# Kernel optimization log

Hardware: AMD Instinct MI355X
Metric: run time of the kernel (lower is better)

## Reference

```python
import jax, jax.numpy as jnp
import numpy as np

D_MODEL = 1024
NUM_HEADS = 16
D_K = D_MODEL // NUM_HEADS
HEADS_DIST = [4, 4, 2, 2, 4]  # [token, statement, data_flow, control_flow, standard]
HYP_DF = 5.0
HYP_CF = 5.0
NEG_INF = -1000000000.0
B, S = 4, 1024


def _head_group_weights():
    # one-hot-per-group weight vectors of length NUM_HEADS
    ws = []
    start = 0
    for n in HEADS_DIST:
        w = np.zeros(NUM_HEADS, dtype=np.float32)
        w[start:start + n] = 1.0
        ws.append(jnp.asarray(w))
        start += n
    return ws  # tok_w, stmt_w, df_w, cf_w, std_w


def setup_inputs() -> dict:
    key = jax.random.key(0)
    ks = jax.random.split(key, 12)
    f32 = jnp.float32
    inp = {
        'Q': jax.random.normal(ks[0], (B, S, D_MODEL), f32),
        'K': jax.random.normal(ks[1], (B, S, D_MODEL), f32),
        'V': jax.random.normal(ks[2], (B, S, D_MODEL), f32),
        'token': jax.random.randint(ks[3], (B, S, S), 0, 2).astype(f32),
        'statement': jax.random.randint(ks[4], (B, S, S), 0, 2).astype(f32),
        'data_flow': jax.random.randint(ks[5], (B, S, S), 0, 2).astype(f32),
        'control_flow': jax.random.randint(ks[6], (B, S, S), 0, 2).astype(f32),
        'zero_matrix': jnp.zeros((B, S, S), f32),
        'mask': jax.random.randint(ks[7], (B, 1, S, S), 0, 2).astype(jnp.int32),
        # linear layer params (torch nn.Linear: y = x @ W.T + b)
        'Wq': jax.random.normal(ks[8], (D_MODEL, D_MODEL), f32) * 0.02,
        'bq': jnp.zeros((D_MODEL,), f32),
        'Wk': jax.random.normal(ks[9], (D_MODEL, D_MODEL), f32) * 0.02,
        'bk': jnp.zeros((D_MODEL,), f32),
        'Wv': jax.random.normal(ks[10], (D_MODEL, D_MODEL), f32) * 0.02,
        'bv': jnp.zeros((D_MODEL,), f32),
        'Wo': jax.random.normal(ks[11], (D_MODEL, D_MODEL), f32) * 0.02,
        'bo': jnp.zeros((D_MODEL,), f32),
    }
    return inp


def _split_heads(x):
    b, s, _ = x.shape
    return x.reshape(b, s, NUM_HEADS, D_K).transpose(0, 2, 1, 3)  # (B,H,S,dk)


def reference(Q, K, V, token, statement, data_flow, control_flow, zero_matrix,
              mask, Wq, bq, Wk, bk, Wv, bv, Wo, bo):
    tok_w, stmt_w, df_w, cf_w, _ = _head_group_weights()

    Qh = _split_heads(Q @ Wq.T + bq)
    Kh = _split_heads(K @ Wk.T + bk)
    Vh = _split_heads(V @ Wv.T + bv)

    scores = jnp.einsum('bhqd,bhkd->bhqk', Qh, Kh) / jnp.sqrt(jnp.float32(D_K))

    # local mask: -1e9 * token for token-heads, -1e9 * statement for statement-heads,
    # zero_matrix (zeros) elsewhere — expressed via per-head group weights instead of
    # the original redundant stack.
    w = lambda v: v[None, :, None, None]  # (1,H,1,1)
    local_mask = NEG_INF * (w(tok_w) * token[:, None] + w(stmt_w) * statement[:, None])
    # global enhance: |scores * (hyp_df*data_flow | hyp_cf*control_flow)| on their heads
    enhance_adj = (HYP_DF * w(df_w) * data_flow[:, None]
                   + HYP_CF * w(cf_w) * control_flow[:, None])
    global_enhance = jnp.abs(enhance_adj * scores)

    scores = scores + local_mask + global_enhance
    scores = jnp.where(mask == 0, NEG_INF, scores)

    probs = jax.nn.softmax(scores, axis=-1)  # (B,H,S,S)
    ctx = jnp.einsum('bhqk,bhkd->bhqd', probs, Vh)
    out = ctx.transpose(0, 2, 1, 3).reshape(B, S, D_MODEL)
    return out @ Wo.T + bo
```

## Files before the change

kernel.cpp:

```cpp
#include <hip/hip_runtime.h>
#include <stdint.h>

typedef unsigned short u16;
typedef unsigned int   u32;
typedef unsigned char  u8;
typedef __attribute__((ext_vector_type(4))) float f32x4;
typedef __attribute__((ext_vector_type(8))) __bf16 bf16x8;
typedef __attribute__((ext_vector_type(2))) unsigned int u32x2;
typedef __attribute__((ext_vector_type(4))) unsigned int u32x4;

#define MFMA16(a, b, c) __builtin_amdgcn_mfma_f32_16x16x32_bf16((a), (b), (c), 0, 0, 0)

__device__ __forceinline__ u16 f2bf(float f) {
  u32 u = __float_as_uint(f);
  return (u16)((u + 0x7fffu + ((u >> 16) & 1u)) >> 16);
}

__device__ __forceinline__ void gl_lds16(const void* g, void* l) {
  __builtin_amdgcn_global_load_lds((const __attribute__((address_space(1))) u32*)g,
                                   (__attribute__((address_space(3))) u32*)l, 16, 0, 0);
}

__device__ __forceinline__ u32 cvtpk(float a, float b) {
  u32 r;
  asm("v_cvt_pk_bf16_f32 %0, %1, %2" : "=v"(r) : "v"(a), "v"(b));
  return r;
}

__device__ __forceinline__ float exp2_hw(float x) {
  float r;
  asm("v_exp_f32 %0, %1" : "=v"(r) : "v"(x));
  return r;
}

__device__ __forceinline__ void plswap32(u32& x, u32& y) {
  u32x2 r = __builtin_amdgcn_permlane32_swap(x, y, false, false);
  x = r.x; y = r.y;
}
__device__ __forceinline__ void plswap16(u32& x, u32& y) {
  u32x2 r = __builtin_amdgcn_permlane16_swap(x, y, false, false);
  x = r.x; y = r.y;
}

__device__ __forceinline__ float redmax_lg(float v) {
  u32 x = __float_as_uint(v), y = x;
  plswap16(x, y);
  float m = fmaxf(__uint_as_float(x), __uint_as_float(y));
  u32 a = __float_as_uint(m), b = a;
  plswap32(a, b);
  return fmaxf(__uint_as_float(a), __uint_as_float(b));
}
__device__ __forceinline__ float redsum_lg(float v) {
  u32 x = __float_as_uint(v), y = x;
  plswap16(x, y);
  float m = __uint_as_float(x) + __uint_as_float(y);
  u32 a = __float_as_uint(m), b = a;
  plswap32(a, b);
  return __uint_as_float(a) + __uint_as_float(b);
}

__device__ __forceinline__ u32 pbit(float t, float s, float d, float c, int m) {
  const u32 nm = (m == 0) ? 1u : 0u;
  u32 r = (t != 0.0f ? 1u : 0u) | (s != 0.0f ? 2u : 0u) | (d != 0.0f ? 4u : 0u) |
          (c != 0.0f ? 8u : 0u) | ((1u - nm) << 4);
  r |= (((t != 0.0f ? 1u : 0u) | nm) << 5) | (((s != 0.0f ? 1u : 0u) | nm) << 6) | (nm << 7);
  return r;
}

__global__ void __launch_bounds__(256) pack_kernel(const float4* __restrict__ tok, const float4* __restrict__ st,
                                                   const float4* __restrict__ df, const float4* __restrict__ cf,
                                                   const int4* __restrict__ msk, u32* __restrict__ pko) {
  const int i = blockIdx.x * 256 + threadIdx.x;
  const int b = i >> 18, rem = i & 262143, q = rem >> 8, k4 = rem & 255;
  const int t = k4 >> 4, nk = (k4 >> 2) & 3, lg = k4 & 3;
  const u32 widx = ((u32)(b * 64 + (q >> 4)) * 16 + t) * 256 + (q & 15) * 16 + lg * 4 + nk;
  float4 vt = tok[i], vs = st[i], vd = df[i], vc = cf[i];
  int4 vm = msk[i];
  u32 b0 = pbit(vt.x, vs.x, vd.x, vc.x, vm.x);
  u32 b1 = pbit(vt.y, vs.y, vd.y, vc.y, vm.y);
  u32 b2 = pbit(vt.z, vs.z, vd.z, vc.z, vm.z);
  u32 b3 = pbit(vt.w, vs.w, vd.w, vc.w, vm.w);
  pko[widx] = b0 | (b1 << 8) | (b2 << 16) | (b3 << 24);
}

__global__ void __launch_bounds__(256) gemm_qkv(const float* __restrict__ Qf, const float* __restrict__ Kf,
                                                const float* __restrict__ Vf, const float* __restrict__ Wqf,
                                                const float* __restrict__ Wkf, const float* __restrict__ Wvf,
                                                const float* __restrict__ bq, const float* __restrict__ bk,
                                                const float* __restrict__ bv, u16* __restrict__ Obase) {
  __shared__ u16 smA[128 * 32];
  __shared__ u16 smB[128 * 32];
  const int fb = blockIdx.x;
  const int lid = (fb & 7) * 96 + (fb >> 3);
  const int z = lid >> 8;
  const int m0 = ((lid & 255) >> 3) * 128;
  const int n0 = (lid & 7) * 128;
  const float* A = (z == 0) ? Qf : (z == 1) ? Kf : Vf;
  const float* W = (z == 0) ? Wqf : (z == 1) ? Wkf : Wvf;
  const float* bias = (z == 0) ? bq : (z == 1) ? bk : bv;
  u16* Out = Obase + (size_t)z * 4194304;
  const int t = threadIdx.x;
  const int w = t >> 6, l = t & 63;
  const int l15 = l & 15, lg = l >> 4;
  const int wr = w >> 1, wc = w & 1;
  f32x4 acc[4][4] = {};
  const int srow = w * 16 + (l >> 2);
  const int scol = (l & 3) * 8;
  const float* Ab = A + (size_t)(m0 + srow) * 1024 + scol;
  const float* Wb = W + (size_t)(n0 + srow) * 1024 + scol;
  u16* sA0 = smA + srow * 32 + scol;
  u16* sB0 = smB + srow * 32 + scol;

  float4 ra[2][2], rb[2][2];
#pragma unroll
  for (int p = 0; p < 2; p++)
#pragma unroll
    for (int hf = 0; hf < 2; hf++) {
      ra[p][hf] = *(const float4*)(Ab + p * 65536 + hf * 4);
      rb[p][hf] = *(const float4*)(Wb + p * 65536 + hf * 4);
    }

  for (int kk = 0; kk < 1024; kk += 32) {
    __syncthreads();
#pragma unroll
    for (int p = 0; p < 2; p++) {
      u32x4 wa = {cvtpk(ra[p][0].x, ra[p][0].y), cvtpk(ra[p][0].z, ra[p][0].w),
                  cvtpk(ra[p][1].x, ra[p][1].y), cvtpk(ra[p][1].z, ra[p][1].w)};
      *(u32x4*)(sA0 + p * 2048) = wa;
      u32x4 wb2 = {cvtpk(rb[p][0].x, rb[p][0].y), cvtpk(rb[p][0].z, rb[p][0].w),
                   cvtpk(rb[p][1].x, rb[p][1].y), cvtpk(rb[p][1].z, rb[p][1].w)};
      *(u32x4*)(sB0 + p * 2048) = wb2;
    }
    __syncthreads();
    if (kk < 992) {
#pragma unroll
      for (int p = 0; p < 2; p++)
#pragma unroll
        for (int hf = 0; hf < 2; hf++) {
          ra[p][hf] = *(const float4*)(Ab + kk + 32 + p * 65536 + hf * 4);
          rb[p][hf] = *(const float4*)(Wb + kk + 32 + p * 65536 + hf * 4);
        }
    }
    bf16x8 af[4], bv_[4];
#pragma unroll
    for (int i = 0; i < 4; i++) af[i] = *(const bf16x8*)(smA + (wr * 64 + i * 16 + l15) * 32 + lg * 8);
#pragma unroll
    for (int i = 0; i < 4; i++) bv_[i] = *(const bf16x8*)(smB + (wc * 64 + i * 16 + l15) * 32 + lg * 8);
#pragma unroll
    for (int i = 0; i < 4; i++)
#pragma unroll
      for (int j = 0; j < 4; j++) acc[i][j] = MFMA16(af[i], bv_[j], acc[i][j]);
  }
#pragma unroll
  for (int j = 0; j < 4; j++) {
    const int n = n0 + wc * 64 + j * 16 + l15;
    const float bvj = bias[n];
#pragma unroll
    for (int i = 0; i < 4; i++) {
      const int mbase = m0 + wr * 64 + i * 16 + lg * 4;
      if (z < 2) {
#pragma unroll
        for (int r = 0; r < 4; r++) {
          const int m = mbase + r;
          Out[((size_t)((m >> 10) * 16 + (n >> 6)) << 16) + (size_t)(m & 1023) * 64 + (n & 63)] =
              f2bf(acc[i][j][r] + bvj);
        }
      } else {
        size_t off = ((size_t)((mbase >> 10) * 16 + (n >> 6)) << 16) + (size_t)(n & 63) * 1024 + (mbase & 1023);
        *(ushort4*)(Out + off) = make_ushort4(f2bf(acc[i][j][0] + bvj), f2bf(acc[i][j][1] + bvj),
                                              f2bf(acc[i][j][2] + bvj), f2bf(acc[i][j][3] + bvj));
      }
    }
  }
}

__global__ void __launch_bounds__(256) gemm_out(const u16* __restrict__ A, const float* __restrict__ W,
                                                const float* __restrict__ bias, float* __restrict__ Out) {
  __shared__ u16 smA[128 * 32];
  __shared__ u16 smB[128 * 32];
  const int fb = blockIdx.x;
  const int lid = (fb & 7) * 32 + (fb >> 3);
  const int m0 = (lid >> 3) * 128;
  const int n0 = (lid & 7) * 128;
  const int t = threadIdx.x;
  const int w = t >> 6, l = t & 63;
  const int l15 = l & 15, lg = l >> 4;
  const int wr = w >> 1, wc = w & 1;
  f32x4 acc[4][4] = {};
  const int srow = w * 16 + (l >> 2);
  const int scol = (l & 3) * 8;
  const u16* Ab = A + (size_t)(m0 + srow) * 1024 + scol;
  const float* Wb = W + (size_t)(n0 + srow) * 1024 + scol;
  u16* sA0 = smA + srow * 32 + scol;
  u16* sB0 = smB + srow * 32 + scol;

  float4 rb[2][2];
#pragma unroll
  for (int p = 0; p < 2; p++)
#pragma unroll
    for (int hf = 0; hf < 2; hf++) rb[p][hf] = *(const float4*)(Wb + p * 65536 + hf * 4);

  for (int kk = 0; kk < 1024; kk += 32) {
    __syncthreads();
    gl_lds16(Ab + kk, sA0);
    gl_lds16(Ab + kk + (size_t)64 * 1024, sA0 + 64 * 32);
#pragma unroll
    for (int p = 0; p < 2; p++) {
      u32x4 wb2 = {cvtpk(rb[p][0].x, rb[p][0].y), cvtpk(rb[p][0].z, rb[p][0].w),
                   cvtpk(rb[p][1].x, rb[p][1].y), cvtpk(rb[p][1].z, rb[p][1].w)};
      *(u32x4*)(sB0 + p * 2048) = wb2;
    }
    __syncthreads();
    if (kk < 992) {
#pragma unroll
      for (int p = 0; p < 2; p++)
#pragma unroll
        for (int hf = 0; hf < 2; hf++) rb[p][hf] = *(const float4*)(Wb + kk + 32 + p * 65536 + hf * 4);
    }
    bf16x8 af[4], bv_[4];
#pragma unroll
    for (int i = 0; i < 4; i++) af[i] = *(const bf16x8*)(smA + (wr * 64 + i * 16 + l15) * 32 + lg * 8);
#pragma unroll
    for (int i = 0; i < 4; i++) bv_[i] = *(const bf16x8*)(smB + (wc * 64 + i * 16 + l15) * 32 + lg * 8);
#pragma unroll
    for (int i = 0; i < 4; i++)
#pragma unroll
      for (int j = 0; j < 4; j++) acc[i][j] = MFMA16(af[i], bv_[j], acc[i][j]);
  }
#pragma unroll
  for (int j = 0; j < 4; j++) {
    const int n = n0 + wc * 64 + j * 16 + l15;
    const float bvj = bias[n];
#pragma unroll
    for (int i = 0; i < 4; i++) {
      const int mbase = m0 + wr * 64 + i * 16 + lg * 4;
#pragma unroll
      for (int r = 0; r < 4; r++) Out[(size_t)(mbase + r) * 1024 + n] = acc[i][j][r] + bvj;
    }
  }
}

__global__ void __launch_bounds__(256) attn_kernel(const u16* __restrict__ Qp, const u16* __restrict__ Kp,
                                                   const u16* __restrict__ Vt, const u8* __restrict__ pack,
                                                   u16* __restrict__ ctx) {
  __shared__ u16 smK[2][4096];
  __shared__ u16 smV[2][4096];
  const float SCL  = 0.18033688011112042f;
  const float NEGL = -1.44269504e9f;
  const int tid = threadIdx.x;
  const int w = tid >> 6, l = tid & 63;
  const int l15 = l & 15, lg = l >> 4;
  const int f = blockIdx.x;
  const int swz = (f & 7) * 128 + (f >> 3);
  const int bh = swz >> 4, bx = swz & 15;
  const int b = bh >> 4, h = bh & 15;
  const int q0 = bx * 64 + w * 16;
  const bool enh = (h >= 8 && h < 12);
  const u32 kbit = (h < 4) ? 0x20u : (h < 8) ? 0x40u : 0x80u;
  const u32 ebit = (h < 10) ? 0x04u : 0x08u;
  const u32 kb_[4] = {kbit, kbit << 8, kbit << 16, kbit << 24};
  const u32 eb_[4] = {ebit, ebit << 8, ebit << 16, ebit << 24};
  const size_t hb = (size_t)bh << 16;

  bf16x8 qf[2];
#pragma unroll
  for (int ks = 0; ks < 2; ks++)
    qf[ks] = *(const bf16x8*)(Qp + hb + (size_t)(q0 + l15) * 64 + ks * 32 + lg * 8);

  const int srow = w * 16 + (l >> 3);
  const int schunk = (l & 7) ^ (l >> 3);
  const u16* Ksrc = Kp + hb + (size_t)srow * 64 + schunk * 8;
  const u16* Vsrc = Vt + hb + (size_t)srow * 1024 + schunk * 8;
  const int c0 = (lg ^ (l15 & 7)) * 8;
  const u8* pkq = pack + ((size_t)((b * 64 + bx * 4 + w) * 16)) * 1024 + (l15 * 4 + lg) * 16;

  gl_lds16(Ksrc, &smK[0][w * 1024]);
  gl_lds16(Ksrc + 512, &smK[0][w * 1024 + 512]);
  gl_lds16(Vsrc, &smV[0][w * 1024]);
  gl_lds16(Vsrc + 8192, &smV[0][w * 1024 + 512]);
  uint4 pk_next = *(const uint4*)(pkq);

  f32x4 octx[4] = {};
  float mrun = -3.0e38f, lrun = 0.0f;

  for (int t = 0; t < 16; t++) {
    __syncthreads();
    const uint4 pkc = pk_next;
    if (t < 15) {
      const int kb = (t + 1) * 64;
      const int nb = (t + 1) & 1;
      gl_lds16(Ksrc + (size_t)kb * 64, &smK[nb][w * 1024]);
      gl_lds16(Ksrc + (size_t)kb * 64 + 512, &smK[nb][w * 1024 + 512]);
      gl_lds16(Vsrc + kb, &smV[nb][w * 1024]);
      gl_lds16(Vsrc + kb + 8192, &smV[nb][w * 1024 + 512]);
      pk_next = *(const uint4*)(pkq + (t + 1) * 1024);
    }
    const u16* bK = smK[t & 1];
    const u16* bV = smV[t & 1];
    f32x4 sc[4];
#pragma unroll
    for (int nk = 0; nk < 4; nk++) {
      const u16* kr = bK + (nk * 16 + l15) * 64;
      bf16x8 kf0 = *(const bf16x8*)(kr + c0);
      bf16x8 kf1 = *(const bf16x8*)(kr + (c0 ^ 32));
      f32x4 z = {0.0f, 0.0f, 0.0f, 0.0f};
      z = MFMA16(kf0, qf[0], z);
      z = MFMA16(kf1, qf[1], z);
      sc[nk] = z;
    }
    const u32 pkw[4] = {pkc.x, pkc.y, pkc.z, pkc.w};
#pragma unroll
    for (int nk = 0; nk < 4; nk++)
#pragma unroll
      for (int r = 0; r < 4; r++) {
        float s = sc[nk][r] * SCL;
        if (enh) s = (pkw[nk] & eb_[r]) ? __builtin_fmaf(fabsf(s), 5.0f, s) : s;
        sc[nk][r] = (pkw[nk] & kb_[r]) ? NEGL : s;
      }
    float mx[4];
#pragma unroll
    for (int nk = 0; nk < 4; nk++)
      mx[nk] = fmaxf(fmaxf(sc[nk][0], sc[nk][1]), fmaxf(sc[nk][2], sc[nk][3]));
    float smax = fmaxf(fmaxf(mx[0], mx[1]), fmaxf(mx[2], mx[3]));
    smax = redmax_lg(smax);
    const bool defer = __all(smax - mrun <= 11.0f);
    const float mn = defer ? mrun : fmaxf(mrun, smax);
    float psum = 0.0f;
#pragma unroll
    for (int nk = 0; nk < 4; nk++)
#pragma unroll
      for (int r = 0; r < 4; r++) {
        float p = exp2_hw(sc[nk][r] - mn);
        sc[nk][r] = p;
        psum += p;
      }
    psum = redsum_lg(psum);
    if (defer) {
      lrun += psum;
    } else {
      const float so = exp2_hw(mrun - mn);
      lrun = lrun * so + psum;
      mrun = mn;
#pragma unroll
      for (int nd = 0; nd < 4; nd++)
#pragma unroll
        for (int r = 0; r < 4; r++) octx[nd][r] *= so;
    }
#pragma unroll
    for (int kk = 0; kk < 2; kk++) {
      u32 a0 = cvtpk(sc[2 * kk][0], sc[2 * kk][1]);
      u32 a1 = cvtpk(sc[2 * kk][2], sc[2 * kk][3]);
      u32 b0 = cvtpk(sc[2 * kk + 1][0], sc[2 * kk + 1][1]);
      u32 b1 = cvtpk(sc[2 * kk + 1][2], sc[2 * kk + 1][3]);
      plswap32(a0, b0);
      plswap32(a1, b1);
      plswap16(a0, b0);
      plswap16(a1, b1);
      u32x4 wv = {a0, a1, b0, b1};
      bf16x8 pfrag = __builtin_bit_cast(bf16x8, wv);
#pragma unroll
      for (int nd = 0; nd < 4; nd++) {
        bf16x8 vf = *(const bf16x8*)(bV + (nd * 16 + l15) * 64 + (c0 ^ (kk * 32)));
        octx[nd] = MFMA16(vf, pfrag, octx[nd]);
      }
    }
  }
  const float inv = 1.0f / lrun;
  u16* cb = ctx + (size_t)b * 1048576 + (size_t)(q0 + l15) * 1024 + h * 64 + lg * 4;
#pragma unroll
  for (int nd = 0; nd < 4; nd++) {
    *(ushort4*)(cb + nd * 16) = make_ushort4(f2bf(octx[nd][0] * inv), f2bf(octx[nd][1] * inv),
                                             f2bf(octx[nd][2] * inv), f2bf(octx[nd][3] * inv));
  }
}

extern "C" void kernel_launch(void* const* d_in, const int* in_sizes, int n_in,
                              void* d_out, int out_size, void* d_ws, size_t ws_size,
                              hipStream_t stream) {
  (void)in_sizes; (void)n_in; (void)out_size; (void)ws_size;
  const float* Q  = (const float*)d_in[0];
  const float* K  = (const float*)d_in[1];
  const float* V  = (const float*)d_in[2];
  const float* tok = (const float*)d_in[3];
  const float* st  = (const float*)d_in[4];
  const float* df  = (const float*)d_in[5];
  const float* cf  = (const float*)d_in[6];
  const int*   msk = (const int*)d_in[8];
  const float* Wq = (const float*)d_in[9];
  const float* bq = (const float*)d_in[10];
  const float* Wk = (const float*)d_in[11];
  const float* bk = (const float*)d_in[12];
  const float* Wv = (const float*)d_in[13];
  const float* bv = (const float*)d_in[14];
  const float* Wo = (const float*)d_in[15];
  const float* bo = (const float*)d_in[16];

  char* ws = (char*)d_ws;
  const size_t MB = 1ull << 20;
  u8*  pkQ = (u8*)(ws);
  u16* Qh  = (u16*)(ws + 4 * MB);
  u16* ctx = (u16*)(ws + 28 * MB);

  pack_kernel<<<4096, 256, 0, stream>>>((const float4*)tok, (const float4*)st, (const float4*)df,
                                        (const float4*)cf, (const int4*)msk, (u32*)pkQ);
  gemm_qkv<<<768, 256, 0, stream>>>(Q, K, V, Wq, Wk, Wv, bq, bk, bv, Qh);
  attn_kernel<<<1024, 256, 0, stream>>>(Qh, Qh + 4194304, Qh + 8388608, pkQ, ctx);
  gemm_out<<<256, 256, 0, stream>>>(ctx, Wo, bo, (float*)d_out);
}
```

Before: 139.4 us.

## Double-buffer LDS in projection GEMMs with padded rows and two-stage prefetch

Both projection GEMMs now ping-pong between two LDS buffers, so stores for the next k-tile overlap with MFMA on the current tile. The explicit barriers and sched_barriers replace the two __syncthreads per iteration. LDS rows are padded from 32 to 36 elements to reduce bank conflicts on the bf16x8 fragment reads. gemm_out drops global_load_lds in favour of register-staged uint4 loads, and the extra prefetch stage raises register pressure and doubles the LDS footprint.

```diff
diff --git a/kernel.cpp b/kernel.cpp
--- a/kernel.cpp
+++ b/kernel.cpp
@@ -10,6 +10,9 @@
 typedef __attribute__((ext_vector_type(4))) unsigned int u32x4;
 
 #define MFMA16(a, b, c) __builtin_amdgcn_mfma_f32_16x16x32_bf16((a), (b), (c), 0, 0, 0)
+#define SBAR() __builtin_amdgcn_s_barrier()
+#define SCHED() __builtin_amdgcn_sched_barrier(0)
+#define LGKM0() asm volatile("s_waitcnt lgkmcnt(0)" ::: "memory")
 
 __device__ __forceinline__ u16 f2bf(float f) {
   u32 u = __float_as_uint(f);
@@ -88,8 +91,8 @@
                                                 const float* __restrict__ Wkf, const float* __restrict__ Wvf,
                                                 const float* __restrict__ bq, const float* __restrict__ bk,
                                                 const float* __restrict__ bv, u16* __restrict__ Obase) {
-  __shared__ u16 smA[128 * 32];
-  __shared__ u16 smB[128 * 32];
+  __shared__ u16 smA[2][128 * 36];
+  __shared__ u16 smB[2][128 * 36];
   const int fb = blockIdx.x;
   const int lid = (fb & 7) * 96 + (fb >> 3);
   const int z = lid >> 8;
@@ -99,8 +102,8 @@
   const float* W = (z == 0) ? Wqf : (z == 1) ? Wkf : Wvf;
   const float* bias = (z == 0) ? bq : (z == 1) ? bk : bv;
   u16* Out = Obase + (size_t)z * 4194304;
-  const int t = threadIdx.x;
-  const int w = t >> 6, l = t & 63;
+  const int tid = threadIdx.x;
+  const int w = tid >> 6, l = tid & 63;
   const int l15 = l & 15, lg = l >> 4;
   const int wr = w >> 1, wc = w & 1;
   f32x4 acc[4][4] = {};
@@ -108,8 +111,7 @@
   const int scol = (l & 3) * 8;
   const float* Ab = A + (size_t)(m0 + srow) * 1024 + scol;
   const float* Wb = W + (size_t)(n0 + srow) * 1024 + scol;
-  u16* sA0 = smA + srow * 32 + scol;
-  u16* sB0 = smB + srow * 32 + scol;
+  const int soff = srow * 36 + scol;
 
   float4 ra[2][2], rb[2][2];
 #pragma unroll
@@ -119,37 +121,65 @@
       ra[p][hf] = *(const float4*)(Ab + p * 65536 + hf * 4);
       rb[p][hf] = *(const float4*)(Wb + p * 65536 + hf * 4);
     }
-
-  for (int kk = 0; kk < 1024; kk += 32) {
-    __syncthreads();
-#pragma unroll
-    for (int p = 0; p < 2; p++) {
-      u32x4 wa = {cvtpk(ra[p][0].x, ra[p][0].y), cvtpk(ra[p][0].z, ra[p][0].w),
-                  cvtpk(ra[p][1].x, ra[p][1].y), cvtpk(ra[p][1].z, ra[p][1].w)};
-      *(u32x4*)(sA0 + p * 2048) = wa;
-      u32x4 wb2 = {cvtpk(rb[p][0].x, rb[p][0].y), cvtpk(rb[p][0].z, rb[p][0].w),
-                   cvtpk(rb[p][1].x, rb[p][1].y), cvtpk(rb[p][1].z, rb[p][1].w)};
-      *(u32x4*)(sB0 + p * 2048) = wb2;
-    }
-    __syncthreads();
-    if (kk < 992) {
-#pragma unroll
-      for (int p = 0; p < 2; p++)
-#pragma unroll
-        for (int hf = 0; hf < 2; hf++) {
-          ra[p][hf] = *(const float4*)(Ab + kk + 32 + p * 65536 + hf * 4);
-          rb[p][hf] = *(const float4*)(Wb + kk + 32 + p * 65536 + hf * 4);
-        }
-    }
+#pragma unroll
+  for (int p = 0; p < 2; p++) {
+    u32x4 wa = {cvtpk(ra[p][0].x, ra[p][0].y), cvtpk(ra[p][0].z, ra[p][0].w),
+                cvtpk(ra[p][1].x, ra[p][1].y), cvtpk(ra[p][1].z, ra[p][1].w)};
+    *(u32x4*)(&smA[0][soff + p * 2304]) = wa;
+    u32x4 wb2 = {cvtpk(rb[p][0].x, rb[p][0].y), cvtpk(rb[p][0].z, rb[p][0].w),
+                 cvtpk(rb[p][1].x, rb[p][1].y), cvtpk(rb[p][1].z, rb[p][1].w)};
+    *(u32x4*)(&smB[0][soff + p * 2304]) = wb2;
+  }
+#pragma unroll
+  for (int p = 0; p < 2; p++)
+#pragma unroll
+    for (int hf = 0; hf < 2; hf++) {
+      ra[p][hf] = *(const float4*)(Ab + 32 + p * 65536 + hf * 4);
+      rb[p][hf] = *(const float4*)(Wb + 32 + p * 65536 + hf * 4);
+    }
+  LGKM0();
+  SBAR();
+
+  for (int it = 0; it < 32; it++) {
+    SCHED();
+    const u16* bA = smA[it & 1];
+    const u16* bB = smB[it & 1];
     bf16x8 af[4], bv_[4];
 #pragma unroll
-    for (int i = 0; i < 4; i++) af[i] = *(const bf16x8*)(smA + (wr * 64 + i * 16 + l15) * 32 + lg * 8);
-#pragma unroll
-    for (int i = 0; i < 4; i++) bv_[i] = *(const bf16x8*)(smB + (wc * 64 + i * 16 + l15) * 32 + lg * 8);
+    for (int i = 0; i < 4; i++) af[i] = *(const bf16x8*)(bA + (wr * 64 + i * 16 + l15) * 36 + lg * 8);
+#pragma unroll
+    for (int i = 0; i < 4; i++) bv_[i] = *(const bf16x8*)(bB + (wc * 64 + i * 16 + l15) * 36 + lg * 8);
 #pragma unroll
     for (int i = 0; i < 4; i++)
 #pragma unroll
       for (int j = 0; j < 4; j++) acc[i][j] = MFMA16(af[i], bv_[j], acc[i][j]);
+    SBAR();
+    SCHED();
+    if (it < 31) {
+      const int nb = (it + 1) & 1;
+#pragma unroll
+      for (int p = 0; p < 2; p++) {
+        u32x4 wa = {cvtpk(ra[p][0].x, ra[p][0].y), cvtpk(ra[p][0].z, ra[p][0].w),
+                    cvtpk(ra[p][1].x, ra[p][1].y), cvtpk(ra[p][1].z, ra[p][1].w)};
+        *(u32x4*)(&smA[nb][soff + p * 2304]) = wa;
+        u32x4 wb2 = {cvtpk(rb[p][0].x, rb[p][0].y), cvtpk(rb[p][0].z, rb[p][0].w),
+                     cvtpk(rb[p][1].x, rb[p][1].y), cvtpk(rb[p][1].z, rb[p][1].w)};
+        *(u32x4*)(&smB[nb][soff + p * 2304]) = wb2;
+      }
+      if (it < 30) {
+        const int kk = (it + 2) * 32;
+#pragma unroll
+        for (int p = 0; p < 2; p++)
+#pragma unroll
+          for (int hf = 0; hf < 2; hf++) {
+            ra[p][hf] = *(const float4*)(Ab + kk + p * 65536 + hf * 4);
+            rb[p][hf] = *(const float4*)(Wb + kk + p * 65536 + hf * 4);
+          }
+      }
+    }
+    LGKM0();
+    SCHED();
+    SBAR();
   }
 #pragma unroll
   for (int j = 0; j < 4; j++) {
@@ -176,14 +206,14 @@
 
 __global__ void __launch_bounds__(256) gemm_out(const u16* __restrict__ A, const float* __restrict__ W,
                                                 const float* __restrict__ bias, float* __restrict__ Out) {
-  __shared__ u16 smA[128 * 32];
-  __shared__ u16 smB[128 * 32];
+  __shared__ u16 smA[2][128 * 36];
+  __shared__ u16 smB[2][128 * 36];
   const int fb = blockIdx.x;
   const int lid = (fb & 7) * 32 + (fb >> 3);
   const int m0 = (lid >> 3) * 128;
   const int n0 = (lid & 7) * 128;
-  const int t = threadIdx.x;
-  const int w = t >> 6, l = t & 63;
+  const int tid = threadIdx.x;
+  const int w = tid >> 6, l = tid & 63;
   const int l15 = l & 15, lg = l >> 4;
   const int wr = w >> 1, wc = w & 1;
   f32x4 acc[4][4] = {};
@@ -191,41 +221,69 @@
   const int scol = (l & 3) * 8;
   const u16* Ab = A + (size_t)(m0 + srow) * 1024 + scol;
   const float* Wb = W + (size_t)(n0 + srow) * 1024 + scol;
-  u16* sA0 = smA + srow * 32 + scol;
-  u16* sB0 = smB + srow * 32 + scol;
-
+  const int soff = srow * 36 + scol;
+
+  uint4 ua[2];
   float4 rb[2][2];
 #pragma unroll
-  for (int p = 0; p < 2; p++)
+  for (int p = 0; p < 2; p++) {
+    ua[p] = *(const uint4*)(Ab + p * 65536);
 #pragma unroll
     for (int hf = 0; hf < 2; hf++) rb[p][hf] = *(const float4*)(Wb + p * 65536 + hf * 4);
-
-  for (int kk = 0; kk < 1024; kk += 32) {
-    __syncthreads();
-    gl_lds16(Ab + kk, sA0);
-    gl_lds16(Ab + kk + (size_t)64 * 1024, sA0 + 64 * 32);
-#pragma unroll
-    for (int p = 0; p < 2; p++) {
-      u32x4 wb2 = {cvtpk(rb[p][0].x, rb[p][0].y), cvtpk(rb[p][0].z, rb[p][0].w),
-                   cvtpk(rb[p][1].x, rb[p][1].y), cvtpk(rb[p][1].z, rb[p][1].w)};
-      *(u32x4*)(sB0 + p * 2048) = wb2;
-    }
-    __syncthreads();
-    if (kk < 992) {
-#pragma unroll
-      for (int p = 0; p < 2; p++)
-#pragma unroll
-        for (int hf = 0; hf < 2; hf++) rb[p][hf] = *(const float4*)(Wb + kk + 32 + p * 65536 + hf * 4);
-    }
+  }
+#pragma unroll
+  for (int p = 0; p < 2; p++) {
+    *(uint4*)(&smA[0][soff + p * 2304]) = ua[p];
+    u32x4 wb2 = {cvtpk(rb[p][0].x, rb[p][0].y), cvtpk(rb[p][0].z, rb[p][0].w),
+                 cvtpk(rb[p][1].x, rb[p][1].y), cvtpk(rb[p][1].z, rb[p][1].w)};
+    *(u32x4*)(&smB[0][soff + p * 2304]) = wb2;
+  }
+#pragma unroll
+  for (int p = 0; p < 2; p++) {
+    ua[p] = *(const uint4*)(Ab + 32 + p * 65536);
+#pragma unroll
+    for (int hf = 0; hf < 2; hf++) rb[p][hf] = *(const float4*)(Wb + 32 + p * 65536 + hf * 4);
+  }
+  LGKM0();
+  SBAR();
+
+  for (int it = 0; it < 32; it++) {
+    SCHED();
+    const u16* bA = smA[it & 1];
+    const u16* bB = smB[it & 1];
     bf16x8 af[4], bv_[4];
 #pragma unroll
-    for (int i = 0; i < 4; i++) af[i] = *(const bf16x8*)(smA + (wr * 64 + i * 16 + l15) * 32 + lg * 8);
-#pragma unroll
-    for (int i = 0; i < 4; i++) bv_[i] = *(const bf16x8*)(smB + (wc * 64 + i * 16 + l15) * 32 + lg * 8);
+    for (int i = 0; i < 4; i++) af[i] = *(const bf16x8*)(bA + (wr * 64 + i * 16 + l15) * 36 + lg * 8);
+#pragma unroll
+    for (int i = 0; i < 4; i++) bv_[i] = *(const bf16x8*)(bB + (wc * 64 + i * 16 + l15) * 36 + lg * 8);
 #pragma unroll
     for (int i = 0; i < 4; i++)
 #pragma unroll
       for (int j = 0; j < 4; j++) acc[i][j] = MFMA16(af[i], bv_[j], acc[i][j]);
+    SBAR();
+    SCHED();
+    if (it < 31) {
+      const int nb = (it + 1) & 1;
+#pragma unroll
+      for (int p = 0; p < 2; p++) {
+        *(uint4*)(&smA[nb][soff + p * 2304]) = ua[p];
+        u32x4 wb2 = {cvtpk(rb[p][0].x, rb[p][0].y), cvtpk(rb[p][0].z, rb[p][0].w),
+                     cvtpk(rb[p][1].x, rb[p][1].y), cvtpk(rb[p][1].z, rb[p][1].w)};
+        *(u32x4*)(&smB[nb][soff + p * 2304]) = wb2;
+      }
+      if (it < 30) {
+        const int kk = (it + 2) * 32;
+#pragma unroll
+        for (int p = 0; p < 2; p++) {
+          ua[p] = *(const uint4*)(Ab + kk + p * 65536);
+#pragma unroll
+          for (int hf = 0; hf < 2; hf++) rb[p][hf] = *(const float4*)(Wb + kk + p * 65536 + hf * 4);
+        }
+      }
+    }
+    LGKM0();
+    SCHED();
+    SBAR();
   }
 #pragma unroll
   for (int j = 0; j < 4; j++) {
```

New measurement: 218.5 us. 56.8% more time.
